# Kernel optimization log

Hardware: AMD Instinct MI355X
Metric: run time of the kernel (lower is better)

Reference implementation:

```python
import jax, jax.numpy as jnp
from jax import lax
import numpy as np

LRELU = 0.01

def conv(x, w, b=None, stride=1, pad=0):
    y = lax.conv_general_dilated(x, w, (stride, stride), [(pad, pad), (pad, pad)],
                                 dimension_numbers=('NCHW', 'OIHW', 'NCHW'))
    return y if b is None else y + b[None, :, None, None]

def deconv(x, w, b, stride=2, pad=1):
    # torch ConvTranspose2d (w: [Cin, Cout, k, k]) == lhs-dilated conv with flipped kernel
    k = w.shape[2]
    wf = jnp.transpose(jnp.flip(w, (2, 3)), (1, 0, 2, 3))  # -> OIHW
    y = lax.conv_general_dilated(x, wf, (1, 1), [(k - 1 - pad, k - 1 - pad)] * 2,
                                 lhs_dilation=(stride, stride),
                                 dimension_numbers=('NCHW', 'OIHW', 'NCHW'))
    return y + b[None, :, None, None]

def bn(x, g, b, eps=1e-5):
    # training-mode BatchNorm2d: batch statistics over (N, H, W)
    m = x.mean((0, 2, 3), keepdims=True)
    v = x.var((0, 2, 3), keepdims=True)
    return (x - m) * lax.rsqrt(v + eps) * g[None, :, None, None] + b[None, :, None, None]

def resblock(x, w1, g1, b1, w2, g2, b2):
    h = jax.nn.relu(bn(conv(x, w1, pad=1), g1, b1))
    return x + bn(conv(h, w2), g2, b2)

def vq_quantize(z, emb, beta=0.25):
    zt = jnp.transpose(z, (0, 2, 3, 1))              # [B,H,W,D]
    D = zt.shape[-1]
    flat = zt.reshape(-1, D)                         # [M,D]
    dist = ((flat ** 2).sum(1, keepdims=True) + (emb ** 2).sum(1)
            - 2.0 * flat @ emb.T)                    # [M,K]
    idx = jnp.argmin(dist, axis=1)                   # [M]
    q = emb[idx].reshape(zt.shape)                   # gather == one-hot @ emb
    loss = beta * jnp.mean((lax.stop_gradient(q) - zt) ** 2)
    q_st = zt + lax.stop_gradient(q - zt)            # straight-through estimator
    counts = jnp.zeros((emb.shape[0],), flat.dtype).at[idx].add(1.0)
    probs = counts / flat.shape[0]
    perplexity = jnp.exp(-jnp.sum(probs * jnp.log(probs + 1e-10)))
    return jnp.transpose(q_st, (0, 3, 1, 2)), loss, perplexity

def vqvae_forward(p, x):
    h = jax.nn.leaky_relu(conv(x, p['e1w'], p['e1b'], 2, 1), LRELU)
    h = jax.nn.leaky_relu(conv(h, p['e2w'], p['e2b'], 2, 1), LRELU)
    h = jax.nn.leaky_relu(conv(h, p['e3w'], p['e3b'], 1, 1), LRELU)
    h = resblock(h, p['er1w'], p['er1g'], p['er1b'], p['er2w'], p['er2g'], p['er2b'])
    h = jax.nn.leaky_relu(h, LRELU)
    encoded = jax.nn.leaky_relu(conv(h, p['e4w'], p['e4b']), LRELU)
    quantized, vq_loss, _ = vq_quantize(encoded, p['emb'])
    h = jax.nn.leaky_relu(conv(quantized, p['d1w'], p['d1b'], 1, 1), LRELU)
    h = resblock(h, p['dr1w'], p['dr1g'], p['dr1b'], p['dr2w'], p['dr2g'], p['dr2b'])
    h = jax.nn.leaky_relu(h, LRELU)
    h = jax.nn.leaky_relu(deconv(h, p['dt1w'], p['dt1b']), LRELU)
    recon = jnp.tanh(deconv(h, p['dt2w'], p['dt2b']))
    return recon, quantized, encoded, vq_loss

def setup_inputs():
    key = jax.random.key(0)
    ks = iter(jax.random.split(key, 40))
    def w(shape, s=0.05):
        return jax.random.normal(next(ks), shape, jnp.float32) * s
    D, K = 64, 512
    return {
        'x': jax.random.normal(next(ks), (64, 3, 128, 128), jnp.float32),
        'e1w': w((32, 3, 4, 4)), 'e1b': jnp.zeros((32,), jnp.float32),
        'e2w': w((64, 32, 4, 4)), 'e2b': jnp.zeros((64,), jnp.float32),
        'e3w': w((64, 64, 3, 3)), 'e3b': jnp.zeros((64,), jnp.float32),
        'er1w': w((64, 64, 3, 3)), 'er1g': jnp.ones((64,), jnp.float32), 'er1b': jnp.zeros((64,), jnp.float32),
        'er2w': w((64, 64, 1, 1)), 'er2g': jnp.ones((64,), jnp.float32), 'er2b': jnp.zeros((64,), jnp.float32),
        'e4w': w((D, 64, 1, 1)), 'e4b': jnp.zeros((D,), jnp.float32),
        'emb': jax.random.normal(next(ks), (K, D), jnp.float32),
        'd1w': w((64, D, 3, 3)), 'd1b': jnp.zeros((64,), jnp.float32),
        'dr1w': w((64, 64, 3, 3)), 'dr1g': jnp.ones((64,), jnp.float32), 'dr1b': jnp.zeros((64,), jnp.float32),
        'dr2w': w((64, 64, 1, 1)), 'dr2g': jnp.ones((64,), jnp.float32), 'dr2b': jnp.zeros((64,), jnp.float32),
        'dt1w': w((64, 32, 4, 4)), 'dt1b': jnp.zeros((32,), jnp.float32),
        'dt2w': w((32, 3, 4, 4)), 'dt2b': jnp.zeros((3,), jnp.float32),
    }

def reference(x, e1w, e1b, e2w, e2b, e3w, e3b, er1w, er1g, er1b, er2w, er2g, er2b,
              e4w, e4b, emb, d1w, d1b, dr1w, dr1g, dr1b, dr2w, dr2g, dr2b,
              dt1w, dt1b, dt2w, dt2b):
    p = dict(e1w=e1w, e1b=e1b, e2w=e2w, e2b=e2b, e3w=e3w, e3b=e3b,
             er1w=er1w, er1g=er1g, er1b=er1b, er2w=er2w, er2g=er2g, er2b=er2b,
             e4w=e4w, e4b=e4b, emb=emb, d1w=d1w, d1b=d1b,
             dr1w=dr1w, dr1g=dr1g, dr1b=dr1b, dr2w=dr2w, dr2g=dr2g, dr2b=dr2b,
             dt1w=dt1w, dt1b=dt1b, dt2w=dt2w, dt2b=dt2b)
    return vqvae_forward(p, x)
```

## Files before the change

### kernel.cpp

```cpp
#include <hip/hip_runtime.h>
#include <math.h>

#define LREL 0.01f
__device__ __forceinline__ float lrelu(float x) { return x > 0.f ? x : LREL * x; }
__device__ __forceinline__ float fast_tanh(float x) {
    x = fminf(fmaxf(x, -10.f), 10.f);
    float a = __expf(2.f * x);
    return (a - 1.f) / (a + 1.f);
}
__device__ __forceinline__ unsigned short f2bf(float f) {
    unsigned u = __float_as_uint(f);
    unsigned r = u + 0x7FFFu + ((u >> 16) & 1u);
    return (unsigned short)(r >> 16);
}
__device__ __forceinline__ float bf2f(unsigned short h) {
    return __uint_as_float(((unsigned)h) << 16);
}

typedef __attribute__((ext_vector_type(8))) short short8;
typedef __attribute__((ext_vector_type(4))) float f32x4;

__global__ void __launch_bounds__(256) conv_e1_t(
    const float* __restrict__ x, const float* __restrict__ w,
    const float* __restrict__ bias,
    unsigned short* __restrict__ outH, unsigned short* __restrict__ outL)
{
    __shared__ float lin[3][18][131];
    __shared__ float lw[3][16][16];
    int b = blockIdx.x;
    int n = b & 63, t = b >> 6;
    int rt = t & 7, cg = t >> 3;
    int tid = threadIdx.x;
    int r = tid >> 5, g = tid & 31;
    const float* inp = x + (size_t)n * 3 * 16384;

    #pragma unroll
    for (int ci = 0; ci < 3; ++ci)
        if (tid < 36) lin[ci][tid >> 1][(tid & 1) ? 129 : 0] = 0.f;
    #pragma unroll
    for (int ci = 0; ci < 3; ++ci)
        #pragma unroll
        for (int k = 0; k < 9; ++k) {
            int idx = k * 256 + tid;
            int row = idx >> 7, col = idx & 127;
            int gy = 16 * rt - 1 + row;
            float v = 0.f;
            if (gy >= 0 && gy < 128)
                v = inp[ci * 16384 + gy * 128 + col];
            lin[ci][row][col + 1] = v;
        }
    for (int i = tid; i < 768; i += 256) {
        int ci = i >> 8, rr = i & 255, co = rr >> 4, tt = rr & 15;
        lw[ci][co][tt] = w[((cg * 16 + co) * 3 + ci) * 16 + tt];
    }
    __syncthreads();

    float acc[16][2];
    #pragma unroll
    for (int co = 0; co < 16; ++co) { acc[co][0] = acc[co][1] = 0.f; }

    #pragma unroll
    for (int ci = 0; ci < 3; ++ci) {
        float win[4][6];
        #pragma unroll
        for (int ky = 0; ky < 4; ++ky)
            #pragma unroll
            for (int dx = 0; dx < 6; ++dx)
                win[ky][dx] = lin[ci][2 * r + ky][4 * g + dx];
        #pragma unroll
        for (int co = 0; co < 16; ++co) {
            #pragma unroll
            for (int ky = 0; ky < 4; ++ky)
                #pragma unroll
                for (int kx = 0; kx < 4; ++kx) {
                    float wv = lw[ci][co][ky * 4 + kx];
                    acc[co][0] = fmaf(win[ky][kx],     wv, acc[co][0]);
                    acc[co][1] = fmaf(win[ky][kx + 2], wv, acc[co][1]);
                }
        }
    }
    int oy = 8 * rt + r;
    size_t base0 = (((size_t)n * 4096 + oy * 64 + 2 * g) * 32 + cg * 16);
    unsigned h0[8], l0[8], h1[8], l1[8];
    #pragma unroll
    for (int p = 0; p < 8; ++p) {
        float bva = bias[cg * 16 + 2 * p];
        float bvb = bias[cg * 16 + 2 * p + 1];
        float va0 = lrelu(acc[2 * p][0] + bva),     vb0 = lrelu(acc[2 * p + 1][0] + bvb);
        float va1 = lrelu(acc[2 * p][1] + bva),     vb1 = lrelu(acc[2 * p + 1][1] + bvb);
        unsigned short ha0 = f2bf(va0), hb0 = f2bf(vb0);
        unsigned short ha1 = f2bf(va1), hb1 = f2bf(vb1);
        h0[p] = (unsigned)ha0 | ((unsigned)hb0 << 16);
        h1[p] = (unsigned)ha1 | ((unsigned)hb1 << 16);
        l0[p] = (unsigned)f2bf(va0 - bf2f(ha0)) | ((unsigned)f2bf(vb0 - bf2f(hb0)) << 16);
        l1[p] = (unsigned)f2bf(va1 - bf2f(ha1)) | ((unsigned)f2bf(vb1 - bf2f(hb1)) << 16);
    }
    unsigned* oH0 = (unsigned*)(outH + base0);
    unsigned* oL0 = (unsigned*)(outL + base0);
    unsigned* oH1 = (unsigned*)(outH + base0 + 32);
    unsigned* oL1 = (unsigned*)(outL + base0 + 32);
    #pragma unroll
    for (int p = 0; p < 8; ++p) {
        oH0[p] = h0[p]; oL0[p] = l0[p];
        oH1[p] = h1[p]; oL1[p] = l1[p];
    }
}

__global__ void __launch_bounds__(512) mfma_e2_k(
    const unsigned short* __restrict__ inH, const unsigned short* __restrict__ inL,
    const float* __restrict__ w, const float* __restrict__ bias,
    unsigned short* __restrict__ outH, unsigned short* __restrict__ outL)
{
    __shared__ unsigned short lEH[18][34][8], lEL[18][34][8];
    __shared__ unsigned short lOH[18][34][8], lOL[18][34][8];
    __shared__ unsigned short lwH[64][136], lwL[64][136];
    int b = blockIdx.x;
    int n = b >> 2, rq = b & 3;
    int tid = threadIdx.x;
    int wv = tid >> 6, l = tid & 63;
    int l15 = l & 15, lhi = l >> 4;

    f32x4 acc[4][2];
    #pragma unroll
    for (int ct = 0; ct < 4; ++ct)
        #pragma unroll
        for (int pt = 0; pt < 2; ++pt) {
            f32x4 z = {0.f, 0.f, 0.f, 0.f};
            acc[ct][pt] = z;
        }

    for (int cc = 0; cc < 4; ++cc) {
        __syncthreads();
        for (int i = tid; i < 1188; i += 512) {
            int row = i / 66, rem = i % 66;
            int par = rem & 1, cp = rem >> 1;
            int gy = 16 * rq - 1 + row;
            int gx = 2 * cp - 1 + par;
            uint4 vH = make_uint4(0u, 0u, 0u, 0u);
            uint4 vL = make_uint4(0u, 0u, 0u, 0u);
            if (gy >= 0 && gy < 64 && gx >= 0 && gx < 64) {
                size_t gi = (((size_t)n * 4096 + gy * 64 + gx) * 32 + cc * 8);
                vH = *(const uint4*)(inH + gi);
                vL = *(const uint4*)(inL + gi);
            }
            if (par == 0) {
                *(uint4*)&lEH[row][cp][0] = vH;
                *(uint4*)&lEL[row][cp][0] = vL;
            } else {
                *(uint4*)&lOH[row][cp][0] = vH;
                *(uint4*)&lOL[row][cp][0] = vL;
            }
        }
        for (int i = tid; i < 8192; i += 512) {
            int co = i >> 7, rr = i & 127;
            int ky = rr >> 5, kx = (rr >> 3) & 3, j = rr & 7;
            float wv0 = w[(co * 32 + cc * 8 + j) * 16 + ky * 4 + kx];
            unsigned short h = f2bf(wv0);
            lwH[co][ky * 32 + kx * 8 + j] = h;
            lwL[co][ky * 32 + kx * 8 + j] = f2bf(wv0 - bf2f(h));
        }
        __syncthreads();

        #pragma unroll
        for (int kg = 0; kg < 4; ++kg) {
            short8 bH[2], bL[2];
            int cpo = lhi >> 1;
            int row = 2 * wv + kg;
            #pragma unroll
            for (int pt = 0; pt < 2; ++pt) {
                int cpp = pt * 16 + l15 + cpo;
                if (lhi & 1) {
                    bH[pt] = *(const short8*)&lOH[row][cpp][0];
                    bL[pt] = *(const short8*)&lOL[row][cpp][0];
                } else {
                    bH[pt] = *(const short8*)&lEH[row][cpp][0];
                    bL[pt] = *(const short8*)&lEL[row][cpp][0];
                }
            }
            #pragma unroll
            for (int ct = 0; ct < 4; ++ct) {
                short8 aH = *(const short8*)&lwH[ct * 16 + l15][kg * 32 + lhi * 8];
                short8 aL = *(const short8*)&lwL[ct * 16 + l15][kg * 32 + lhi * 8];
                #pragma unroll
                for (int pt = 0; pt < 2; ++pt) {
                    acc[ct][pt] = __builtin_amdgcn_mfma_f32_16x16x32_bf16(aH, bH[pt], acc[ct][pt], 0, 0, 0);
                    acc[ct][pt] = __builtin_amdgcn_mfma_f32_16x16x32_bf16(aH, bL[pt], acc[ct][pt], 0, 0, 0);
                    acc[ct][pt] = __builtin_amdgcn_mfma_f32_16x16x32_bf16(aL, bH[pt], acc[ct][pt], 0, 0, 0);
                }
            }
        }
    }

    int oy = 8 * rq + wv;
    #pragma unroll
    for (int pt = 0; pt < 2; ++pt) {
        int ox = pt * 16 + l15;
        size_t base = (((size_t)n * 1024 + oy * 32 + ox) << 6);
        #pragma unroll
        for (int ct = 0; ct < 4; ++ct) {
            int co0 = ct * 16 + lhi * 4;
            #pragma unroll
            for (int jp = 0; jp < 2; ++jp) {
                float v0 = lrelu(acc[ct][pt][2 * jp]     + bias[co0 + 2 * jp]);
                float v1 = lrelu(acc[ct][pt][2 * jp + 1] + bias[co0 + 2 * jp + 1]);
                unsigned short h0 = f2bf(v0), h1 = f2bf(v1);
                *(unsigned*)(outH + base + co0 + 2 * jp) = (unsigned)h0 | ((unsigned)h1 << 16);
                *(unsigned*)(outL + base + co0 + 2 * jp) =
                    (unsigned)f2bf(v0 - bf2f(h0)) | ((unsigned)f2bf(v1 - bf2f(h1)) << 16);
            }
        }
    }
}

template<int IN, int ACT, int STATS>
__global__ void __launch_bounds__(256) conv1x1_t(
    const float* __restrict__ in, const float* __restrict__ res,
    const float* __restrict__ w, const float* __restrict__ bias,
    const float* __restrict__ fin, const float* __restrict__ g,
    const float* __restrict__ beta, float* __restrict__ out,
    float* __restrict__ psum, float* __restrict__ pss)
{
    __shared__ float lw[64][64];
    __shared__ float sga[64], sbb[64];
    int b = blockIdx.x;
    int n = b >> 3, pxb = b & 7;
    int tid = threadIdx.x;
    int pxg = tid & 31, cog = tid >> 5;
    for (int i = tid; i < 4096; i += 256) {
        int co = i >> 6, ci = i & 63;
        lw[ci][co] = w[co * 64 + ci];
    }
    if (IN >= 1 && tid < 64) {
        float ga = g[tid] * fin[2 * tid + 1];
        sga[tid] = ga;
        sbb[tid] = beta[tid] - fin[2 * tid] * ga;
    }
    __syncthreads();

    size_t base = (size_t)n * 65536 + pxb * 128 + pxg * 4;
    float acc[8][4];
    #pragma unroll
    for (int co = 0; co < 8; ++co) { acc[co][0]=acc[co][1]=acc[co][2]=acc[co][3]=0.f; }
    #pragma unroll 4
    for (int ci = 0; ci < 64; ++ci) {
        float4 xv = *(const float4*)(in + base + (size_t)ci * 1024);
        float x0, x1, x2, x3;
        if (IN == 1) {
            float ga = sga[ci], bb = sbb[ci];
            x0 = fmaxf(fmaf(xv.x, ga, bb), 0.f);
            x1 = fmaxf(fmaf(xv.y, ga, bb), 0.f);
            x2 = fmaxf(fmaf(xv.z, ga, bb), 0.f);
            x3 = fmaxf(fmaf(xv.w, ga, bb), 0.f);
        } else if (IN == 2) {
            float4 rv = *(const float4*)(res + base + (size_t)ci * 1024);
            float ga = sga[ci], bb = sbb[ci];
            x0 = lrelu(rv.x + fmaf(xv.x, ga, bb));
            x1 = lrelu(rv.y + fmaf(xv.y, ga, bb));
            x2 = lrelu(rv.z + fmaf(xv.z, ga, bb));
            x3 = lrelu(rv.w + fmaf(xv.w, ga, bb));
        } else {
            x0 = xv.x; x1 = xv.y; x2 = xv.z; x3 = xv.w;
        }
        const float4* wr = (const float4*)&lw[ci][cog * 8];
        float4 wa = wr[0], wb = wr[1];
        acc[0][0] = fmaf(x0, wa.x, acc[0][0]); acc[0][1] = fmaf(x1, wa.x, acc[0][1]);
        acc[0][2] = fmaf(x2, wa.x, acc[0][2]); acc[0][3] = fmaf(x3, wa.x, acc[0][3]);
        acc[1][0] = fmaf(x0, wa.y, acc[1][0]); acc[1][1] = fmaf(x1, wa.y, acc[1][1]);
        acc[1][2] = fmaf(x2, wa.y, acc[1][2]); acc[1][3] = fmaf(x3, wa.y, acc[1][3]);
        acc[2][0] = fmaf(x0, wa.z, acc[2][0]); acc[2][1] = fmaf(x1, wa.z, acc[2][1]);
        acc[2][2] = fmaf(x2, wa.z, acc[2][2]); acc[2][3] = fmaf(x3, wa.z, acc[2][3]);
        acc[3][0] = fmaf(x0, wa.w, acc[3][0]); acc[3][1] = fmaf(x1, wa.w, acc[3][1]);
        acc[3][2] = fmaf(x2, wa.w, acc[3][2]); acc[3][3] = fmaf(x3, wa.w, acc[3][3]);
        acc[4][0] = fmaf(x0, wb.x, acc[4][0]); acc[4][1] = fmaf(x1, wb.x, acc[4][1]);
        acc[4][2] = fmaf(x2, wb.x, acc[4][2]); acc[4][3] = fmaf(x3, wb.x, acc[4][3]);
        acc[5][0] = fmaf(x0, wb.y, acc[5][0]); acc[5][1] = fmaf(x1, wb.y, acc[5][1]);
        acc[5][2] = fmaf(x2, wb.y, acc[5][2]); acc[5][3] = fmaf(x3, wb.y, acc[5][3]);
        acc[6][0] = fmaf(x0, wb.z, acc[6][0]); acc[6][1] = fmaf(x1, wb.z, acc[6][1]);
        acc[6][2] = fmaf(x2, wb.z, acc[6][2]); acc[6][3] = fmaf(x3, wb.z, acc[6][3]);
        acc[7][0] = fmaf(x0, wb.w, acc[7][0]); acc[7][1] = fmaf(x1, wb.w, acc[7][1]);
        acc[7][2] = fmaf(x2, wb.w, acc[7][2]); acc[7][3] = fmaf(x3, wb.w, acc[7][3]);
    }
    #pragma unroll
    for (int co = 0; co < 8; ++co) {
        int coG = cog * 8 + co;
        float bv = bias ? bias[coG] : 0.f;
        float a0 = acc[co][0] + bv, a1 = acc[co][1] + bv, a2 = acc[co][2] + bv, a3 = acc[co][3] + bv;
        if (ACT == 1) { a0 = lrelu(a0); a1 = lrelu(a1); a2 = lrelu(a2); a3 = lrelu(a3); }
        float4 v; v.x = a0; v.y = a1; v.z = a2; v.w = a3;
        *(float4*)(out + base + (size_t)coG * 1024) = v;
        if (STATS) {
            float s = a0 + a1 + a2 + a3;
            float q = a0*a0 + a1*a1 + a2*a2 + a3*a3;
            #pragma unroll
            for (int m = 1; m < 32; m <<= 1) {
                s += __shfl_xor(s, m);
                q += __shfl_xor(q, m);
            }
            if (pxg == 0) {
                psum[(size_t)coG * 512 + n * 8 + pxb] = s;
                pss [(size_t)coG * 512 + n * 8 + pxb] = q;
            }
        }
    }
}

__global__ void bn_fin2_k(const float* __restrict__ psum, const float* __restrict__ pss,
                          float* __restrict__ fin, float invM, int cnt)
{
    __shared__ float s1[64][4], s2[64][4];
    int c = threadIdx.x >> 2, part = threadIdx.x & 3;
    int per = cnt >> 2;
    float s = 0.f, q = 0.f;
    for (int i = part * per; i < (part + 1) * per; ++i) {
        s += psum[(size_t)c * cnt + i];
        q += pss[(size_t)c * cnt + i];
    }
    s1[c][part] = s; s2[c][part] = q;
    __syncthreads();
    if (part == 0) {
        float ss = s1[c][0] + s1[c][1] + s1[c][2] + s1[c][3];
        float qq = s2[c][0] + s2[c][1] + s2[c][2] + s2[c][3];
        float mean = ss * invM;
        float var  = qq * invM - mean * mean;
        fin[2 * c] = mean;
        fin[2 * c + 1] = rsqrtf(var + 1e-5f);
    }
}

__global__ void bn_fin3_k(const float* __restrict__ psum, const float* __restrict__ pss,
                          float* __restrict__ fin, float invM)
{
    int c = threadIdx.x;
    if (c >= 64) return;
    float s = 0.f, q = 0.f;
    for (int i = 0; i < 256; ++i) { s += psum[c * 256 + i]; q += pss[c * 256 + i]; }
    float mean = s * invM;
    float var  = q * invM - mean * mean;
    fin[2 * c] = mean;
    fin[2 * c + 1] = rsqrtf(var + 1e-5f);
}

template<int MODE>
__global__ void __launch_bounds__(256) trans_k(
    const float* __restrict__ in, const float* __restrict__ fin,
    const float* __restrict__ g, const float* __restrict__ beta,
    unsigned short* __restrict__ outT)
{
    __shared__ unsigned short tt[256][68];
    __shared__ float sga[64], sbb[64];
    int b = blockIdx.x;
    int n = b >> 2, pxb = b & 3;
    int tid = threadIdx.x;
    if (MODE == 1) {
        if (tid < 64) {
            float ga = g[tid] * fin[2 * tid + 1];
            sga[tid] = ga;
            sbb[tid] = beta[tid] - fin[2 * tid] * ga;
        }
        __syncthreads();
    }
    for (int i = tid; i < 16384; i += 256) {
        int ci = i >> 8, px = i & 255;
        float v = in[((size_t)(n * 64 + ci) << 10) + pxb * 256 + px];
        if (MODE == 1) v = fmaxf(fmaf(v, sga[ci], sbb[ci]), 0.f);
        tt[px][ci] = f2bf(v);
    }
    __syncthreads();
    for (int o = tid; o < 4096; o += 256) {
        int px = o >> 4, c4 = o & 15;
        uint2 v = *(const uint2*)&tt[px][c4 * 4];
        *(uint2*)(outT + ((((size_t)n << 10) + pxb * 256 + px) << 6) + c4 * 4) = v;
    }
}

template<int INM>
__global__ void __launch_bounds__(256) trans_hl_k(
    const float* __restrict__ inA, const float* __restrict__ inB,
    const float* __restrict__ bias2,
    unsigned short* __restrict__ outH, unsigned short* __restrict__ outL)
{
    __shared__ unsigned short th[256][68];
    __shared__ unsigned short tl[256][68];
    __shared__ float sb[64];
    int b = blockIdx.x;
    int n = b >> 2, pxb = b & 3;
    int tid = threadIdx.x;
    if (INM == 1 && tid < 64) sb[tid] = bias2[tid];
    if (INM == 1) __syncthreads();
    for (int i = tid; i < 16384; i += 256) {
        int ci = i >> 8, px = i & 255;
        size_t gi = ((size_t)(n * 64 + ci) << 10) + pxb * 256 + px;
        float v = inA[gi];
        if (INM == 1) v = lrelu(v + inB[gi] + sb[ci]);
        unsigned short h = f2bf(v);
        th[px][ci] = h;
        tl[px][ci] = f2bf(v - bf2f(h));
    }
    __syncthreads();
    for (int o = tid; o < 4096; o += 256) {
        int px = o >> 4, c4 = o & 15;
        size_t oidx = ((((size_t)n << 10) + pxb * 256 + px) << 6) + c4 * 4;
        *(uint2*)(outH + oidx) = *(const uint2*)&th[px][c4 * 4];
        *(uint2*)(outL + oidx) = *(const uint2*)&tl[px][c4 * 4];
    }
}

__global__ void __launch_bounds__(256) bnres_trans_k(
    const float* __restrict__ xin, const float* __restrict__ res,
    const float* __restrict__ fin, const float* __restrict__ g,
    const float* __restrict__ beta, unsigned short* __restrict__ outT)
{
    __shared__ unsigned short tt[256][68];
    __shared__ float sga[64], sbb[64];
    int b = blockIdx.x;
    int n = b >> 2, pxb = b & 3;
    int tid = threadIdx.x;
    if (tid < 64) {
        float ga = g[tid] * fin[2 * tid + 1];
        sga[tid] = ga;
        sbb[tid] = beta[tid] - fin[2 * tid] * ga;
    }
    __syncthreads();
    for (int i = tid; i < 16384; i += 256) {
        int ci = i >> 8, px = i & 255;
        size_t gi = ((size_t)(n * 64 + ci) << 10) + pxb * 256 + px;
        float v = lrelu(res[gi] + fmaf(xin[gi], sga[ci], sbb[ci]));
        tt[px][ci] = f2bf(v);
    }
    __syncthreads();
    for (int o = tid; o < 4096; o += 256) {
        int px = o >> 4, c4 = o & 15;
        uint2 v = *(const uint2*)&tt[px][c4 * 4];
        *(uint2*)(outT + ((((size_t)n << 10) + pxb * 256 + px) << 6) + c4 * 4) = v;
    }
}

template<int ACT, int STATS>
__global__ void __launch_bounds__(256) mfma_conv3x3_k(
    const unsigned short* __restrict__ inT, const float* __restrict__ w,
    const float* __restrict__ bias, float* __restrict__ out,
    float* __restrict__ psum, float* __restrict__ pss)
{
    __shared__ unsigned short lin[10][34][40];
    __shared__ unsigned short lwA[32][296];
    __shared__ float sS[4][32], sQ[4][32];
    int b = blockIdx.x;
    int cg = b & 1, pxb = (b >> 1) & 3, n = b >> 3;
    int tid = threadIdx.x;
    int wv = tid >> 6, l = tid & 63;
    int l15 = l & 15, lhi = l >> 4;

    f32x4 acc[2][4];
    #pragma unroll
    for (int ct = 0; ct < 2; ++ct)
        #pragma unroll
        for (int bt = 0; bt < 4; ++bt) {
            f32x4 z = {0.f, 0.f, 0.f, 0.f};
            acc[ct][bt] = z;
        }

    for (int c2 = 0; c2 < 2; ++c2) {
        __syncthreads();
        for (int i = tid; i < 1360; i += 256) {
            int pos = i >> 2, q = i & 3;
            int row = pos / 34, col = pos % 34;
            int iy = pxb * 8 - 1 + row, ix = col - 1;
            uint4 v = make_uint4(0u, 0u, 0u, 0u);
            if (iy >= 0 && iy < 32 && ix >= 0 && ix < 32)
                v = *(const uint4*)(inT + ((((size_t)n << 10) + iy * 32 + ix) << 6) + c2 * 32 + q * 8);
            *(uint4*)&lin[row][col][q * 8] = v;
        }
        for (int i = tid; i < 9216; i += 256) {
            int col = i / 288, k = i % 288;
            int tap = k >> 5, cc = k & 31;
            int co = cg * 32 + col;
            lwA[col][k] = f2bf(w[(co * 64 + c2 * 32 + cc) * 9 + tap]);
        }
        __syncthreads();
        #pragma unroll
        for (int tap = 0; tap < 9; ++tap) {
            const int dy = tap / 3, dx = tap % 3;
            short8 a[2], bb[4];
            #pragma unroll
            for (int ct = 0; ct < 2; ++ct)
                a[ct] = *(const short8*)&lwA[ct * 16 + l15][tap * 32 + lhi * 8];
            #pragma unroll
            for (int bt = 0; bt < 4; ++bt) {
                int rr = 2 * wv + (bt >> 1);
                int cc0 = (bt & 1) * 16;
                bb[bt] = *(const short8*)&lin[rr + dy][cc0 + l15 + dx][lhi * 8];
            }
            #pragma unroll
            for (int ct = 0; ct < 2; ++ct)
                #pragma unroll
                for (int bt = 0; bt < 4; ++bt)
                    acc[ct][bt] = __builtin_amdgcn_mfma_f32_16x16x32_bf16(a[ct], bb[bt], acc[ct][bt], 0, 0, 0);
        }
    }

    int orow0 = pxb * 8 + 2 * wv;
    #pragma unroll
    for (int ct = 0; ct < 2; ++ct) {
        #pragma unroll
        for (int j = 0; j < 4; ++j) {
            int co_l = ct * 16 + lhi * 4 + j;
            int co = cg * 32 + co_l;
            float bv = bias ? bias[co] : 0.f;
            float s = 0.f, q = 0.f;
            #pragma unroll
            for (int bt = 0; bt < 4; ++bt) {
                float v = acc[ct][bt][j] + bv;
                if (ACT == 1) v = lrelu(v);
                int row = orow0 + (bt >> 1);
                int col = (bt & 1) * 16 + l15;
                out[(((size_t)n * 64 + co) << 10) + row * 32 + col] = v;
                if (STATS) { s += v; q = fmaf(v, v, q); }
            }
            if (STATS) {
                #pragma unroll
                for (int m = 1; m < 16; m <<= 1) {
                    s += __shfl_xor(s, m);
                    q += __shfl_xor(q, m);
                }
                if (l15 == 0) { sS[wv][co_l] = s; sQ[wv][co_l] = q; }
            }
        }
    }
    if (STATS) {
        __syncthreads();
        if (tid < 32) {
            float s = sS[0][tid] + sS[1][tid] + sS[2][tid] + sS[3][tid];
            float q = sQ[0][tid] + sQ[1][tid] + sQ[2][tid] + sQ[3][tid];
            psum[(cg * 32 + tid) * 256 + n * 4 + pxb] = s;
            pss [(cg * 32 + tid) * 256 + n * 4 + pxb] = q;
        }
    }
}

template<int ACT, int STATS>
__global__ void __launch_bounds__(256) mfma_conv3x3_hl_k(
    const unsigned short* __restrict__ inH, const unsigned short* __restrict__ inL,
    const float* __restrict__ w, const float* __restrict__ bias,
    float* __restrict__ out, float* __restrict__ psum, float* __restrict__ pss)
{
    __shared__ unsigned short linH[10][34][40];
    __shared__ unsigned short linL[10][34][40];
    __shared__ unsigned short lwH[32][296];
    __shared__ unsigned short lwL[32][296];
    __shared__ float sS[4][32], sQ[4][32];
    int b = blockIdx.x;
    int cg = b & 1, pxb = (b >> 1) & 3, n = b >> 3;
    int tid = threadIdx.x;
    int wv = tid >> 6, l = tid & 63;
    int l15 = l & 15, lhi = l >> 4;

    f32x4 acc[2][4];
    #pragma unroll
    for (int ct = 0; ct < 2; ++ct)
        #pragma unroll
        for (int bt = 0; bt < 4; ++bt) {
            f32x4 z = {0.f, 0.f, 0.f, 0.f};
            acc[ct][bt] = z;
        }

    for (int c2 = 0; c2 < 2; ++c2) {
        __syncthreads();
        for (int i = tid; i < 1360; i += 256) {
            int pos = i >> 2, q = i & 3;
            int row = pos / 34, col = pos % 34;
            int iy = pxb * 8 - 1 + row, ix = col - 1;
            uint4 vh = make_uint4(0u, 0u, 0u, 0u);
            uint4 vl = make_uint4(0u, 0u, 0u, 0u);
            if (iy >= 0 && iy < 32 && ix >= 0 && ix < 32) {
                size_t gi = ((((size_t)n << 10) + iy * 32 + ix) << 6) + c2 * 32 + q * 8;
                vh = *(const uint4*)(inH + gi);
                vl = *(const uint4*)(inL + gi);
            }
            *(uint4*)&linH[row][col][q * 8] = vh;
            *(uint4*)&linL[row][col][q * 8] = vl;
        }
        for (int i = tid; i < 9216; i += 256) {
            int col = i / 288, k = i % 288;
            int tap = k >> 5, cc = k & 31;
            int co = cg * 32 + col;
            float wv0 = w[(co * 64 + c2 * 32 + cc) * 9 + tap];
            unsigned short h = f2bf(wv0);
            lwH[col][k] = h;
            lwL[col][k] = f2bf(wv0 - bf2f(h));
        }
        __syncthreads();
        #pragma unroll
        for (int tap = 0; tap < 9; ++tap) {
            const int dy = tap / 3, dx = tap % 3;
            short8 aH[2], aL[2], bH[4], bL[4];
            #pragma unroll
            for (int ct = 0; ct < 2; ++ct) {
                aH[ct] = *(const short8*)&lwH[ct * 16 + l15][tap * 32 + lhi * 8];
                aL[ct] = *(const short8*)&lwL[ct * 16 + l15][tap * 32 + lhi * 8];
            }
            #pragma unroll
            for (int bt = 0; bt < 4; ++bt) {
                int rr = 2 * wv + (bt >> 1);
                int cc0 = (bt & 1) * 16;
                bH[bt] = *(const short8*)&linH[rr + dy][cc0 + l15 + dx][lhi * 8];
                bL[bt] = *(const short8*)&linL[rr + dy][cc0 + l15 + dx][lhi * 8];
            }
            #pragma unroll
            for (int ct = 0; ct < 2; ++ct)
                #pragma unroll
                for (int bt = 0; bt < 4; ++bt) {
                    acc[ct][bt] = __builtin_amdgcn_mfma_f32_16x16x32_bf16(aH[ct], bH[bt], acc[ct][bt], 0, 0, 0);
                    acc[ct][bt] = __builtin_amdgcn_mfma_f32_16x16x32_bf16(aH[ct], bL[bt], acc[ct][bt], 0, 0, 0);
                    acc[ct][bt] = __builtin_amdgcn_mfma_f32_16x16x32_bf16(aL[ct], bH[bt], acc[ct][bt], 0, 0, 0);
                }
        }
    }

    int orow0 = pxb * 8 + 2 * wv;
    #pragma unroll
    for (int ct = 0; ct < 2; ++ct) {
        #pragma unroll
        for (int j = 0; j < 4; ++j) {
            int co_l = ct * 16 + lhi * 4 + j;
            int co = cg * 32 + co_l;
            float bv = bias ? bias[co] : 0.f;
            float s = 0.f, q = 0.f;
            #pragma unroll
            for (int bt = 0; bt < 4; ++bt) {
                float v = acc[ct][bt][j] + bv;
                if (ACT == 1) v = lrelu(v);
                int row = orow0 + (bt >> 1);
                int col = (bt & 1) * 16 + l15;
                out[(((size_t)n * 64 + co) << 10) + row * 32 + col] = v;
                if (STATS) { s += v; q = fmaf(v, v, q); }
            }
            if (STATS) {
                #pragma unroll
                for (int m = 1; m < 16; m <<= 1) {
                    s += __shfl_xor(s, m);
                    q += __shfl_xor(q, m);
                }
                if (l15 == 0) { sS[wv][co_l] = s; sQ[wv][co_l] = q; }
            }
        }
    }
    if (STATS) {
        __syncthreads();
        if (tid < 32) {
            float s = sS[0][tid] + sS[1][tid] + sS[2][tid] + sS[3][tid];
            float q = sQ[0][tid] + sQ[1][tid] + sQ[2][tid] + sQ[3][tid];
            psum[(cg * 32 + tid) * 256 + n * 4 + pxb] = s;
            pss [(cg * 32 + tid) * 256 + n * 4 + pxb] = q;
        }
    }
}

template<int ACT, int STATS>
__global__ void __launch_bounds__(256) mfma_conv1x1_k(
    const unsigned short* __restrict__ inT, const float* __restrict__ w,
    const float* __restrict__ bias, float* __restrict__ out,
    float* __restrict__ psum, float* __restrict__ pss)
{
    __shared__ unsigned short lin[256][72];
    __shared__ unsigned short lwA[32][72];
    __shared__ float sS[4][32], sQ[4][32];
    int b = blockIdx.x;
    int cg = b & 1, pxb = (b >> 1) & 3, n = b >> 3;
    int tid = threadIdx.x;
    int wv = tid >> 6, l = tid & 63;
    int l15 = l & 15, lhi = l >> 4;

    for (int i = tid; i < 2048; i += 256) {
        int px = i >> 3, q = i & 7;
        uint4 v = *(const uint4*)(inT + ((((size_t)n << 10) + pxb * 256 + px) << 6) + q * 8);
        *(uint4*)&lin[px][q * 8] = v;
    }
    for (int i = tid; i < 2048; i += 256) {
        int col = i >> 6, ci = i & 63;
        lwA[col][ci] = f2bf(w[(cg * 32 + col) * 64 + ci]);
    }
    __syncthreads();

    f32x4 acc[2][4];
    #pragma unroll
    for (int ct = 0; ct < 2; ++ct)
        #pragma unroll
        for (int bt = 0; bt < 4; ++bt) {
            f32x4 z = {0.f, 0.f, 0.f, 0.f};
            acc[ct][bt] = z;
        }

    #pragma unroll
    for (int ks = 0; ks < 2; ++ks) {
        short8 a[2], bb[4];
        #pragma unroll
        for (int ct = 0; ct < 2; ++ct)
            a[ct] = *(const short8*)&lwA[ct * 16 + l15][ks * 32 + lhi * 8];
        #pragma unroll
        for (int bt = 0; bt < 4; ++bt)
            bb[bt] = *(const short8*)&lin[wv * 64 + bt * 16 + l15][ks * 32 + lhi * 8];
        #pragma unroll
        for (int ct = 0; ct < 2; ++ct)
            #pragma unroll
            for (int bt = 0; bt < 4; ++bt)
                acc[ct][bt] = __builtin_amdgcn_mfma_f32_16x16x32_bf16(a[ct], bb[bt], acc[ct][bt], 0, 0, 0);
    }

    #pragma unroll
    for (int ct = 0; ct < 2; ++ct) {
        #pragma unroll
        for (int j = 0; j < 4; ++j) {
            int co_l = ct * 16 + lhi * 4 + j;
            int co = cg * 32 + co_l;
            float bv = bias ? bias[co] : 0.f;
            float s = 0.f, q = 0.f;
            #pragma unroll
            for (int bt = 0; bt < 4; ++bt) {
                float v = acc[ct][bt][j] + bv;
                if (ACT == 1) v = lrelu(v);
                int px = pxb * 256 + wv * 64 + bt * 16 + l15;
                out[(((size_t)n * 64 + co) << 10) + px] = v;
                if (STATS) { s += v; q = fmaf(v, v, q); }
            }
            if (STATS) {
                #pragma unroll
                for (int m = 1; m < 16; m <<= 1) {
                    s += __shfl_xor(s, m);
                    q += __shfl_xor(q, m);
                }
                if (l15 == 0) { sS[wv][co_l] = s; sQ[wv][co_l] = q; }
            }
        }
    }
    if (STATS) {
        __syncthreads();
        if (tid < 32) {
            float s = sS[0][tid] + sS[1][tid] + sS[2][tid] + sS[3][tid];
            float q = sQ[0][tid] + sQ[1][tid] + sQ[2][tid] + sQ[3][tid];
            psum[(cg * 32 + tid) * 256 + n * 4 + pxb] = s;
            pss [(cg * 32 + tid) * 256 + n * 4 + pxb] = q;
        }
    }
}

__global__ void __launch_bounds__(256) mfma_dt1_k(
    const unsigned short* __restrict__ inT, const float* __restrict__ w,
    const float* __restrict__ bias, float* __restrict__ out)
{
    __shared__ unsigned short lin[5][34][40];
    __shared__ unsigned short lwA[2][32][136];
    int b = blockIdx.x;
    int ublk = b & 7, p_y = (b >> 3) & 1, n = b >> 4;
    int tid = threadIdx.x;
    int wv = tid >> 6, l = tid & 63;
    int l15 = l & 15, lhi = l >> 4;
    int pq = wv & 1;
    int vbase = 1 - pq;
    int ubase = ublk * 4 + (p_y == 0 ? 1 : 0);

    f32x4 acc[2][4];
    #pragma unroll
    for (int ct = 0; ct < 2; ++ct)
        #pragma unroll
        for (int bt = 0; bt < 4; ++bt) {
            f32x4 z = {0.f, 0.f, 0.f, 0.f};
            acc[ct][bt] = z;
        }

    for (int ch = 0; ch < 2; ++ch) {
        __syncthreads();
        for (int i = tid; i < 680; i += 256) {
            int rr = i / 136, rem = i % 136;
            int jc = rem >> 2, q = rem & 3;
            int gy = ubase - 1 + rr, gx = jc - 1;
            uint4 v = make_uint4(0u, 0u, 0u, 0u);
            if (gy >= 0 && gy < 32 && gx >= 0 && gx < 32)
                v = *(const uint4*)(inT + ((((size_t)n << 10) + gy * 32 + gx) << 6) + ch * 32 + q * 8);
            *(uint4*)&lin[rr][jc][q * 8] = v;
        }
        for (int i = tid; i < 8192; i += 256) {
            int pqq = i >> 12, co = (i >> 7) & 31, k = i & 127;
            int tap = k >> 5, cc = k & 31;
            int ci = ch * 32 + cc;
            int ky = p_y + 2 * (tap >> 1), kx = pqq + 2 * (tap & 1);
            lwA[pqq][co][k] = f2bf(w[((ci * 32 + co) << 4) + ky * 4 + kx]);
        }
        __syncthreads();
        #pragma unroll
        for (int ks = 0; ks < 4; ++ks) {
            int ty = ks >> 1, tx = ks & 1;
            short8 a[2], bb[4];
            #pragma unroll
            for (int ct = 0; ct < 2; ++ct)
                a[ct] = *(const short8*)&lwA[pq][ct * 16 + l15][ks * 32 + lhi * 8];
            #pragma unroll
            for (int bt = 0; bt < 4; ++bt) {
                int jloc = (wv >> 1) * 2 + (bt >> 1);
                int vloc = (bt & 1) * 16 + l15;
                bb[bt] = *(const short8*)&lin[jloc + 1 - ty][vloc + vbase + 1 - tx][lhi * 8];
            }
            #pragma unroll
            for (int ct = 0; ct < 2; ++ct)
                #pragma unroll
// ... 159 lines not shown
        float z1 = z[base + (size_t)(d + 1) * 1024];
        float q0 = eb[d], q1 = eb[d + 1];
        out_q[base + (size_t)d * 1024]       = q0;
        out_q[base + (size_t)(d + 1) * 1024] = q1;
        float d0 = q0 - z0, d1 = q1 - z1;
        lsum = fmaf(d0, d0, lsum);
        lsum = fmaf(d1, d1, lsum);
        tq32[tid][d >> 1] = (unsigned)f2bf(q0) | ((unsigned)f2bf(q1) << 16);
    }
    sh[tid] = lsum;
    __syncthreads();
    unsigned* oT = (unsigned*)outT;
    size_t m0 = (size_t)blockIdx.x * 256;
    #pragma unroll
    for (int k = 0; k < 32; ++k) {
        int j = k * 256 + tid;
        int px = j >> 5, c = j & 31;
        oT[(m0 + px) * 32 + c] = tq32[px][c];
    }
    for (int st = 128; st > 0; st >>= 1) {
        if (tid < st) sh[tid] += sh[tid + st];
        __syncthreads();
    }
    if (tid == 0) partials[blockIdx.x] = sh[0];
}

__global__ void vq_fin_k(const float* __restrict__ partials, float* __restrict__ out)
{
    __shared__ float sh[256];
    sh[threadIdx.x] = partials[threadIdx.x];
    __syncthreads();
    for (int st = 128; st > 0; st >>= 1) {
        if (threadIdx.x < st) sh[threadIdx.x] += sh[threadIdx.x + st];
        __syncthreads();
    }
    if (threadIdx.x == 0) out[0] = sh[0] * (0.25f / (65536.f * 64.f));
}

__global__ void __launch_bounds__(256) deconv_dt2_t(
    const float* __restrict__ in, const float* __restrict__ w,
    const float* __restrict__ bias, float* __restrict__ out)
{
    __shared__ float lin[8][4][67];
    __shared__ float lw[8][3][16];
    int b = blockIdx.x;
    int n = b & 63, rt = b >> 6;
    int tid = threadIdx.x;
    int r4 = tid >> 6, g = tid & 63;
    int oy = rt * 4 + r4;
    const float* inp = in + (size_t)n * 32 * 4096;
    int iy0 = 2 * rt - 1;
    int ky0 = (oy + 1) & 1;
    int iyA = ((oy + 1 - ky0) >> 1) - iy0;
    int iyB = iyA - 1;

    if (tid < 64) lin[tid >> 3][(tid >> 1) & 3][(tid & 1) ? 65 : 0] = 0.f;

    float acc[3][2];
    #pragma unroll
    for (int co = 0; co < 3; ++co) { acc[co][0] = acc[co][1] = 0.f; }

    int scol = tid & 63, srs = tid >> 6;
    for (int cic = 0; cic < 4; ++cic) {
        __syncthreads();
        {
            int gy = iy0 + srs;
            bool ok = (gy >= 0 && gy < 64);
            #pragma unroll
            for (int k = 0; k < 8; ++k) {
                float v = ok ? inp[(cic * 8 + k) * 4096 + gy * 64 + scol] : 0.f;
                lin[k][srs][scol + 1] = v;
            }
        }
        if (tid < 128) {
            int ci = tid >> 4, tt = tid & 15;
            #pragma unroll
            for (int co = 0; co < 3; ++co)
                lw[ci][co][tt] = w[((cic * 8 + ci) * 3 + co) * 16 + tt];
        }
        __syncthreads();
        #pragma unroll 2
        for (int ci = 0; ci < 8; ++ci) {
            float vA0 = lin[ci][iyA][g],     vA1 = lin[ci][iyA][g + 1], vA2 = lin[ci][iyA][g + 2];
            float vB0 = lin[ci][iyB][g],     vB1 = lin[ci][iyB][g + 1], vB2 = lin[ci][iyB][g + 2];
            #pragma unroll
            for (int co = 0; co < 3; ++co) {
                const float4* wp = (const float4*)lw[ci][co];
                float4 wA = wp[ky0];
                float4 wB = wp[ky0 + 2];
                acc[co][0] = fmaf(vA1, wA.y, fmaf(vA0, wA.w, fmaf(vB1, wB.y, fmaf(vB0, wB.w, acc[co][0]))));
                acc[co][1] = fmaf(vA2, wA.x, fmaf(vA1, wA.z, fmaf(vB2, wB.x, fmaf(vB1, wB.z, acc[co][1]))));
            }
        }
    }
    #pragma unroll
    for (int co = 0; co < 3; ++co) {
        float bv = bias[co];
        float2 v;
        v.x = fast_tanh(acc[co][0] + bv);
        v.y = fast_tanh(acc[co][1] + bv);
        *(float2*)(out + ((size_t)(n * 3 + co) * 16384) + oy * 128 + 2 * g) = v;
    }
}

extern "C" void kernel_launch(void* const* d_in, const int* in_sizes, int n_in,
                              void* d_out, int out_size, void* d_ws, size_t ws_size,
                              hipStream_t stream)
{
    const float* x    = (const float*)d_in[0];
    const float* e1w  = (const float*)d_in[1];
    const float* e1b  = (const float*)d_in[2];
    const float* e2w  = (const float*)d_in[3];
    const float* e2b  = (const float*)d_in[4];
    const float* e3w  = (const float*)d_in[5];
    const float* e3b  = (const float*)d_in[6];
    const float* er1w = (const float*)d_in[7];
    const float* er1g = (const float*)d_in[8];
    const float* er1b = (const float*)d_in[9];
    const float* er2w = (const float*)d_in[10];
    const float* er2g = (const float*)d_in[11];
    const float* er2b = (const float*)d_in[12];
    const float* e4w  = (const float*)d_in[13];
    const float* e4b  = (const float*)d_in[14];
    const float* emb  = (const float*)d_in[15];
    const float* d1w  = (const float*)d_in[16];
    const float* d1b  = (const float*)d_in[17];
    const float* dr1w = (const float*)d_in[18];
    const float* dr1g = (const float*)d_in[19];
    const float* dr1b = (const float*)d_in[20];
    const float* dr2w = (const float*)d_in[21];
    const float* dr2g = (const float*)d_in[22];
    const float* dr2b = (const float*)d_in[23];
    const float* dt1w = (const float*)d_in[24];
    const float* dt1b = (const float*)d_in[25];
    const float* dt2w = (const float*)d_in[26];
    const float* dt2b = (const float*)d_in[27];

    float* out = (float*)d_out;
    float* ws  = (float*)d_ws;

    float* B0 = ws;
    float* B1 = ws + 8388608;
    float* B2 = B1 + 4194304;
    float* B3 = B2 + 4194304;
    float* B4 = B3 + 4194304;
    float* psum   = B4 + 4194304;
    float* pss    = psum + 32768;
    float* fin    = pss + 32768;
    float* vq_part = fin + 128;
    unsigned long long* bestbuf = (unsigned long long*)(vq_part + 256);
    unsigned short* embH = (unsigned short*)(bestbuf + 65536);
    unsigned short* embL = embH + 32768;
    float* enq = (float*)(embL + 32768);

    unsigned short* e1H  = (unsigned short*)B0;
    unsigned short* e1L  = e1H + 8388608;
    unsigned short* tbuf  = (unsigned short*)B1;
    unsigned short* tbufH = (unsigned short*)B3;
    unsigned short* tbufL = (unsigned short*)B4;

    float* out_recon = out;
    float* out_q     = out + 3145728;
    float* out_e     = out + 7340032;
    float* out_loss  = out + 11534336;

    const float invM = 1.f / 65536.f;

    vq_prep_k<<<128, 256, 0, stream>>>(emb, embH, embL, enq);
    conv_e1_t<<<1024, 256, 0, stream>>>(x, e1w, e1b, e1H, e1L);
    mfma_e2_k<<<256, 512, 0, stream>>>(e1H, e1L, e2w, e2b, tbufH, tbufL);

    mfma_conv3x3_hl_k<1,0><<<512, 256, 0, stream>>>(tbufH, tbufL, e3w, e3b, B2, nullptr, nullptr);

    trans_hl_k<0><<<256, 256, 0, stream>>>(B2, nullptr, nullptr, tbufH, tbufL);
    mfma_conv3x3_hl_k<0,1><<<512, 256, 0, stream>>>(tbufH, tbufL, er1w, nullptr, B1, psum, pss);
    bn_fin3_k<<<1, 64, 0, stream>>>(psum, pss, fin, invM);

    conv1x1_t<1,0,1><<<512, 256, 0, stream>>>(B1, nullptr, er2w, nullptr, fin, er1g, er1b, B4, psum, pss);
    bn_fin2_k<<<1, 256, 0, stream>>>(psum, pss, fin, invM, 512);
    conv1x1_t<2,1,0><<<512, 256, 0, stream>>>(B4, B2, e4w, e4b, fin, er2g, er2b, out_e, nullptr, nullptr);

    vq_dist_mfma_k<<<512, 256, 0, stream>>>(out_e, embH, embL, enq, bestbuf);
    vq_combine_k<<<256, 256, 0, stream>>>(out_e, emb, bestbuf, out_q, tbuf, vq_part);
    vq_fin_k<<<1, 256, 0, stream>>>(vq_part, out_loss);

    mfma_conv3x3_k<1,0><<<512, 256, 0, stream>>>(tbuf, d1w, d1b, B2, nullptr, nullptr);

    trans_k<0><<<256, 256, 0, stream>>>(B2, nullptr, nullptr, nullptr, tbuf);
    mfma_conv3x3_k<0,1><<<512, 256, 0, stream>>>(tbuf, dr1w, nullptr, B3, psum, pss);
    bn_fin3_k<<<1, 64, 0, stream>>>(psum, pss, fin, invM);

    trans_k<1><<<256, 256, 0, stream>>>(B3, fin, dr1g, dr1b, tbuf);
    mfma_conv1x1_k<0,1><<<512, 256, 0, stream>>>(tbuf, dr2w, nullptr, B4, psum, pss);
    bn_fin3_k<<<1, 64, 0, stream>>>(psum, pss, fin, invM);

    bnres_trans_k<<<256, 256, 0, stream>>>(B4, B2, fin, dr2g, dr2b, tbuf);
    mfma_dt1_k<<<1024, 256, 0, stream>>>(tbuf, dt1w, dt1b, B0);

    deconv_dt2_t<<<2048, 256, 0, stream>>>(B0, dt2w, dt2b, out_recon);
}
```

Baseline: 485.8 us.

## Pre-pack conv weights to bf16 once and widen 3x3 conv blocks to 512 threads

Adds a weight-prep kernel that converts the e2, e3, er1, d1 and dr1 weights once into bf16 hi/lo arrays laid out the way the kernels read them. The conv kernels then copy weights into shared memory with 16-byte vector loads instead of doing strided scalar gathers and conversions in every block. The 3x3 MFMA kernels also move to 512 threads with one output row per wave, which halves per-wave accumulators and raises parallelism. This costs an extra kernel launch and more workspace, and the larger blocks may lower occupancy.

```diff
diff --git a/kernel.cpp b/kernel.cpp
--- a/kernel.cpp
+++ b/kernel.cpp
@@ -19,6 +19,43 @@
 
 typedef __attribute__((ext_vector_type(8))) short short8;
 typedef __attribute__((ext_vector_type(4))) float f32x4;
+
+__global__ void __launch_bounds__(256) wprep_k(
+    const float* __restrict__ e3w, const float* __restrict__ er1w,
+    const float* __restrict__ d1w, const float* __restrict__ dr1w,
+    const float* __restrict__ e2w,
+    unsigned short* __restrict__ e3wH, unsigned short* __restrict__ e3wL,
+    unsigned short* __restrict__ er1wH, unsigned short* __restrict__ er1wL,
+    unsigned short* __restrict__ d1wH, unsigned short* __restrict__ dr1wH,
+    unsigned short* __restrict__ e2wH, unsigned short* __restrict__ e2wL)
+{
+    int b = blockIdx.x, tid = threadIdx.x;
+    if (b < 576) {
+        int region = b / 144;
+        int idx = (b % 144) * 256 + tid;
+        int chunk = idx / 9216, r = idx % 9216;
+        int col = r / 288, k = r % 288;
+        int tap = k >> 5, cc = k & 31;
+        int cg = chunk & 1, c2 = chunk >> 1;
+        int co = cg * 32 + col, ci = c2 * 32 + cc;
+        const float* w = region == 0 ? e3w : region == 1 ? er1w : region == 2 ? d1w : dr1w;
+        float v = w[(co * 64 + ci) * 9 + tap];
+        unsigned short h = f2bf(v);
+        if (region == 0)      { e3wH[idx] = h;  e3wL[idx]  = f2bf(v - bf2f(h)); }
+        else if (region == 1) { er1wH[idx] = h; er1wL[idx] = f2bf(v - bf2f(h)); }
+        else if (region == 2) d1wH[idx] = h;
+        else                  dr1wH[idx] = h;
+    } else {
+        int idx = (b - 576) * 256 + tid;
+        int cc = idx >> 13, r = idx & 8191;
+        int co = r >> 7, k = r & 127;
+        int ky = k >> 5, kx = (k >> 3) & 3, j = k & 7;
+        float v = e2w[(co * 32 + cc * 8 + j) * 16 + ky * 4 + kx];
+        unsigned short h = f2bf(v);
+        e2wH[idx] = h;
+        e2wL[idx] = f2bf(v - bf2f(h));
+    }
+}
 
 __global__ void __launch_bounds__(256) conv_e1_t(
     const float* __restrict__ x, const float* __restrict__ w,
@@ -108,7 +145,8 @@
 
 __global__ void __launch_bounds__(512) mfma_e2_k(
     const unsigned short* __restrict__ inH, const unsigned short* __restrict__ inL,
-    const float* __restrict__ w, const float* __restrict__ bias,
+    const unsigned short* __restrict__ wpH, const unsigned short* __restrict__ wpL,
+    const float* __restrict__ bias,
     unsigned short* __restrict__ outH, unsigned short* __restrict__ outL)
 {
     __shared__ unsigned short lEH[18][34][8], lEL[18][34][8];
@@ -151,13 +189,11 @@
                 *(uint4*)&lOL[row][cp][0] = vL;
             }
         }
-        for (int i = tid; i < 8192; i += 512) {
-            int co = i >> 7, rr = i & 127;
-            int ky = rr >> 5, kx = (rr >> 3) & 3, j = rr & 7;
-            float wv0 = w[(co * 32 + cc * 8 + j) * 16 + ky * 4 + kx];
-            unsigned short h = f2bf(wv0);
-            lwH[co][ky * 32 + kx * 8 + j] = h;
-            lwL[co][ky * 32 + kx * 8 + j] = f2bf(wv0 - bf2f(h));
+        for (int i = tid; i < 1024; i += 512) {
+            int co = i >> 4, q = i & 15;
+            size_t gb = (size_t)cc * 8192 + co * 128 + q * 8;
+            *(uint4*)&lwH[co][q * 8] = *(const uint4*)(wpH + gb);
+            *(uint4*)&lwL[co][q * 8] = *(const uint4*)(wpL + gb);
         }
         __syncthreads();
 
@@ -436,32 +472,32 @@
 }
 
 template<int ACT, int STATS>
-__global__ void __launch_bounds__(256) mfma_conv3x3_k(
-    const unsigned short* __restrict__ inT, const float* __restrict__ w,
+__global__ void __launch_bounds__(512) mfma_conv3x3_k(
+    const unsigned short* __restrict__ inT, const unsigned short* __restrict__ wpH,
     const float* __restrict__ bias, float* __restrict__ out,
     float* __restrict__ psum, float* __restrict__ pss)
 {
     __shared__ unsigned short lin[10][34][40];
     __shared__ unsigned short lwA[32][296];
-    __shared__ float sS[4][32], sQ[4][32];
+    __shared__ float sS[8][32], sQ[8][32];
     int b = blockIdx.x;
     int cg = b & 1, pxb = (b >> 1) & 3, n = b >> 3;
     int tid = threadIdx.x;
     int wv = tid >> 6, l = tid & 63;
     int l15 = l & 15, lhi = l >> 4;
 
-    f32x4 acc[2][4];
+    f32x4 acc[2][2];
     #pragma unroll
     for (int ct = 0; ct < 2; ++ct)
         #pragma unroll
-        for (int bt = 0; bt < 4; ++bt) {
+        for (int bt = 0; bt < 2; ++bt) {
             f32x4 z = {0.f, 0.f, 0.f, 0.f};
             acc[ct][bt] = z;
         }
 
     for (int c2 = 0; c2 < 2; ++c2) {
         __syncthreads();
-        for (int i = tid; i < 1360; i += 256) {
+        for (int i = tid; i < 1360; i += 512) {
             int pos = i >> 2, q = i & 3;
             int row = pos / 34, col = pos % 34;
             int iy = pxb * 8 - 1 + row, ix = col - 1;
@@ -470,35 +506,31 @@
                 v = *(const uint4*)(inT + ((((size_t)n << 10) + iy * 32 + ix) << 6) + c2 * 32 + q * 8);
             *(uint4*)&lin[row][col][q * 8] = v;
         }
-        for (int i = tid; i < 9216; i += 256) {
-            int col = i / 288, k = i % 288;
-            int tap = k >> 5, cc = k & 31;
-            int co = cg * 32 + col;
-            lwA[col][k] = f2bf(w[(co * 64 + c2 * 32 + cc) * 9 + tap]);
+        for (int i = tid; i < 1152; i += 512) {
+            int col = i / 36, q = i % 36;
+            size_t gb = (size_t)(c2 * 2 + cg) * 9216 + col * 288 + q * 8;
+            *(uint4*)&lwA[col][q * 8] = *(const uint4*)(wpH + gb);
         }
         __syncthreads();
         #pragma unroll
         for (int tap = 0; tap < 9; ++tap) {
             const int dy = tap / 3, dx = tap % 3;
-            short8 a[2], bb[4];
+            short8 a[2], bb[2];
             #pragma unroll
             for (int ct = 0; ct < 2; ++ct)
                 a[ct] = *(const short8*)&lwA[ct * 16 + l15][tap * 32 + lhi * 8];
             #pragma unroll
-            for (int bt = 0; bt < 4; ++bt) {
-                int rr = 2 * wv + (bt >> 1);
-                int cc0 = (bt & 1) * 16;
-                bb[bt] = *(const short8*)&lin[rr + dy][cc0 + l15 + dx][lhi * 8];
-            }
+            for (int bt = 0; bt < 2; ++bt)
+                bb[bt] = *(const short8*)&lin[wv + dy][bt * 16 + l15 + dx][lhi * 8];
             #pragma unroll
             for (int ct = 0; ct < 2; ++ct)
                 #pragma unroll
-                for (int bt = 0; bt < 4; ++bt)
+                for (int bt = 0; bt < 2; ++bt)
                     acc[ct][bt] = __builtin_amdgcn_mfma_f32_16x16x32_bf16(a[ct], bb[bt], acc[ct][bt], 0, 0, 0);
         }
     }
 
-    int orow0 = pxb * 8 + 2 * wv;
+    int orow = pxb * 8 + wv;
     #pragma unroll
     for (int ct = 0; ct < 2; ++ct) {
         #pragma unroll
@@ -508,12 +540,11 @@
             float bv = bias ? bias[co] : 0.f;
             float s = 0.f, q = 0.f;
             #pragma unroll
-            for (int bt = 0; bt < 4; ++bt) {
+            for (int bt = 0; bt < 2; ++bt) {
                 float v = acc[ct][bt][j] + bv;
                 if (ACT == 1) v = lrelu(v);
-                int row = orow0 + (bt >> 1);
-                int col = (bt & 1) * 16 + l15;
-                out[(((size_t)n * 64 + co) << 10) + row * 32 + col] = v;
+                int col = bt * 16 + l15;
+                out[(((size_t)n * 64 + co) << 10) + orow * 32 + col] = v;
                 if (STATS) { s += v; q = fmaf(v, v, q); }
             }
             if (STATS) {
@@ -529,8 +560,9 @@
     if (STATS) {
         __syncthreads();
         if (tid < 32) {
-            float s = sS[0][tid] + sS[1][tid] + sS[2][tid] + sS[3][tid];
-            float q = sQ[0][tid] + sQ[1][tid] + sQ[2][tid] + sQ[3][tid];
+            float s = 0.f, q = 0.f;
+            #pragma unroll
+            for (int k = 0; k < 8; ++k) { s += sS[k][tid]; q += sQ[k][tid]; }
             psum[(cg * 32 + tid) * 256 + n * 4 + pxb] = s;
             pss [(cg * 32 + tid) * 256 + n * 4 + pxb] = q;
         }
@@ -538,34 +570,35 @@
 }
 
 template<int ACT, int STATS>
-__global__ void __launch_bounds__(256) mfma_conv3x3_hl_k(
+__global__ void __launch_bounds__(512) mfma_conv3x3_hl_k(
     const unsigned short* __restrict__ inH, const unsigned short* __restrict__ inL,
-    const float* __restrict__ w, const float* __restrict__ bias,
+    const unsigned short* __restrict__ wpH, const unsigned short* __restrict__ wpL,
+    const float* __restrict__ bias,
     float* __restrict__ out, float* __restrict__ psum, float* __restrict__ pss)
 {
     __shared__ unsigned short linH[10][34][40];
     __shared__ unsigned short linL[10][34][40];
     __shared__ unsigned short lwH[32][296];
     __shared__ unsigned short lwL[32][296];
-    __shared__ float sS[4][32], sQ[4][32];
+    __shared__ float sS[8][32], sQ[8][32];
     int b = blockIdx.x;
     int cg = b & 1, pxb = (b >> 1) & 3, n = b >> 3;
     int tid = threadIdx.x;
     int wv = tid >> 6, l = tid & 63;
     int l15 = l & 15, lhi = l >> 4;
 
-    f32x4 acc[2][4];
+    f32x4 acc[2][2];
     #pragma unroll
     for (int ct = 0; ct < 2; ++ct)
         #pragma unroll
-        for (int bt = 0; bt < 4; ++bt) {
+        for (int bt = 0; bt < 2; ++bt) {
             f32x4 z = {0.f, 0.f, 0.f, 0.f};
             acc[ct][bt] = z;
         }
 
     for (int c2 = 0; c2 < 2; ++c2) {
         __syncthreads();
-        for (int i = tid; i < 1360; i += 256) {
+        for (int i = tid; i < 1360; i += 512) {
             int pos = i >> 2, q = i & 3;
             int row = pos / 34, col = pos % 34;
             int iy = pxb * 8 - 1 + row, ix = col - 1;
@@ -579,36 +612,31 @@
             *(uint4*)&linH[row][col][q * 8] = vh;
             *(uint4*)&linL[row][col][q * 8] = vl;
         }
-        for (int i = tid; i < 9216; i += 256) {
-            int col = i / 288, k = i % 288;
-            int tap = k >> 5, cc = k & 31;
-            int co = cg * 32 + col;
-            float wv0 = w[(co * 64 + c2 * 32 + cc) * 9 + tap];
-            unsigned short h = f2bf(wv0);
-            lwH[col][k] = h;
-            lwL[col][k] = f2bf(wv0 - bf2f(h));
+        for (int i = tid; i < 1152; i += 512) {
+            int col = i / 36, q = i % 36;
+            size_t gb = (size_t)(c2 * 2 + cg) * 9216 + col * 288 + q * 8;
+            *(uint4*)&lwH[col][q * 8] = *(const uint4*)(wpH + gb);
+            *(uint4*)&lwL[col][q * 8] = *(const uint4*)(wpL + gb);
         }
         __syncthreads();
         #pragma unroll
         for (int tap = 0; tap < 9; ++tap) {
             const int dy = tap / 3, dx = tap % 3;
-            short8 aH[2], aL[2], bH[4], bL[4];
+            short8 aH[2], aL[2], bH[2], bL[2];
             #pragma unroll
             for (int ct = 0; ct < 2; ++ct) {
                 aH[ct] = *(const short8*)&lwH[ct * 16 + l15][tap * 32 + lhi * 8];
                 aL[ct] = *(const short8*)&lwL[ct * 16 + l15][tap * 32 + lhi * 8];
             }
             #pragma unroll
-            for (int bt = 0; bt < 4; ++bt) {
-                int rr = 2 * wv + (bt >> 1);
-                int cc0 = (bt & 1) * 16;
-                bH[bt] = *(const short8*)&linH[rr + dy][cc0 + l15 + dx][lhi * 8];
-                bL[bt] = *(const short8*)&linL[rr + dy][cc0 + l15 + dx][lhi * 8];
+            for (int bt = 0; bt < 2; ++bt) {
+                bH[bt] = *(const short8*)&linH[wv + dy][bt * 16 + l15 + dx][lhi * 8];
+                bL[bt] = *(const short8*)&linL[wv + dy][bt * 16 + l15 + dx][lhi * 8];
             }
             #pragma unroll
             for (int ct = 0; ct < 2; ++ct)
                 #pragma unroll
-                for (int bt = 0; bt < 4; ++bt) {
+                for (int bt = 0; bt < 2; ++bt) {
                     acc[ct][bt] = __builtin_amdgcn_mfma_f32_16x16x32_bf16(aH[ct], bH[bt], acc[ct][bt], 0, 0, 0);
                     acc[ct][bt] = __builtin_amdgcn_mfma_f32_16x16x32_bf16(aH[ct], bL[bt], acc[ct][bt], 0, 0, 0);
                     acc[ct][bt] = __builtin_amdgcn_mfma_f32_16x16x32_bf16(aL[ct], bH[bt], acc[ct][bt], 0, 0, 0);
@@ -616,7 +644,7 @@
         }
     }
 
-    int orow0 = pxb * 8 + 2 * wv;
+    int orow = pxb * 8 + wv;
     #pragma unroll
     for (int ct = 0; ct < 2; ++ct) {
         #pragma unroll
@@ -626,12 +654,11 @@
             float bv = bias ? bias[co] : 0.f;
             float s = 0.f, q = 0.f;
             #pragma unroll
-            for (int bt = 0; bt < 4; ++bt) {
+            for (int bt = 0; bt < 2; ++bt) {
                 float v = acc[ct][bt][j] + bv;
                 if (ACT == 1) v = lrelu(v);
-                int row = orow0 + (bt >> 1);
-                int col = (bt & 1) * 16 + l15;
-                out[(((size_t)n * 64 + co) << 10) + row * 32 + col] = v;
+                int col = bt * 16 + l15;
+                out[(((size_t)n * 64 + co) << 10) + orow * 32 + col] = v;
                 if (STATS) { s += v; q = fmaf(v, v, q); }
             }
             if (STATS) {
@@ -647,8 +674,9 @@
     if (STATS) {
         __syncthreads();
         if (tid < 32) {
-            float s = sS[0][tid] + sS[1][tid] + sS[2][tid] + sS[3][tid];
-            float q = sQ[0][tid] + sQ[1][tid] + sQ[2][tid] + sQ[3][tid];
+            float s = 0.f, q = 0.f;
+            #pragma unroll
+            for (int k = 0; k < 8; ++k) { s += sS[k][tid]; q += sQ[k][tid]; }
             psum[(cg * 32 + tid) * 256 + n * 4 + pxb] = s;
             pss [(cg * 32 + tid) * 256 + n * 4 + pxb] = q;
         }
@@ -1114,6 +1142,14 @@
     unsigned short* embH = (unsigned short*)(bestbuf + 65536);
     unsigned short* embL = embH + 32768;
     float* enq = (float*)(embL + 32768);
+    unsigned short* e3wH  = (unsigned short*)(enq + 512);
+    unsigned short* e3wL  = e3wH + 36864;
+    unsigned short* er1wH = e3wL + 36864;
+    unsigned short* er1wL = er1wH + 36864;
+    unsigned short* d1wH  = er1wL + 36864;
+    unsigned short* dr1wH = d1wH + 36864;
+    unsigned short* e2wH  = dr1wH + 36864;
+    unsigned short* e2wL  = e2wH + 32768;
 
     unsigned short* e1H  = (unsigned short*)B0;
     unsigned short* e1L  = e1H + 8388608;
@@ -1128,14 +1164,17 @@
 
     const float invM = 1.f / 65536.f;
 
+    wprep_k<<<704, 256, 0, stream>>>(e3w, er1w, d1w, dr1w, e2w,
+                                     e3wH, e3wL, er1wH, er1wL, d1wH, dr1wH, e2wH, e2wL);
     vq_prep_k<<<128, 256, 0, stream>>>(emb, embH, embL, enq);
+
     conv_e1_t<<<1024, 256, 0, stream>>>(x, e1w, e1b, e1H, e1L);
-    mfma_e2_k<<<256, 512, 0, stream>>>(e1H, e1L, e2w, e2b, tbufH, tbufL);
-
-    mfma_conv3x3_hl_k<1,0><<<512, 256, 0, stream>>>(tbufH, tbufL, e3w, e3b, B2, nullptr, nullptr);
+    mfma_e2_k<<<256, 512, 0, stream>>>(e1H, e1L, e2wH, e2wL, e2b, tbufH, tbufL);
+
+    mfma_conv3x3_hl_k<1,0><<<512, 512, 0, stream>>>(tbufH, tbufL, e3wH, e3wL, e3b, B2, nullptr, nullptr);
 
     trans_hl_k<0><<<256, 256, 0, stream>>>(B2, nullptr, nullptr, tbufH, tbufL);
-    mfma_conv3x3_hl_k<0,1><<<512, 256, 0, stream>>>(tbufH, tbufL, er1w, nullptr, B1, psum, pss);
+    mfma_conv3x3_hl_k<0,1><<<512, 512, 0, stream>>>(tbufH, tbufL, er1wH, er1wL, nullptr, B1, psum, pss);
     bn_fin3_k<<<1, 64, 0, stream>>>(psum, pss, fin, invM);
 
     conv1x1_t<1,0,1><<<512, 256, 0, stream>>>(B1, nullptr, er2w, nullptr, fin, er1g, er1b, B4, psum, pss);
@@ -1146,10 +1185,10 @@
     vq_combine_k<<<256, 256, 0, stream>>>(out_e, emb, bestbuf, out_q, tbuf, vq_part);
     vq_fin_k<<<1, 256, 0, stream>>>(vq_part, out_loss);
 
-    mfma_conv3x3_k<1,0><<<512, 256, 0, stream>>>(tbuf, d1w, d1b, B2, nullptr, nullptr);
+    mfma_conv3x3_k<1,0><<<512, 512, 0, stream>>>(tbuf, d1wH, d1b, B2, nullptr, nullptr);
 
     trans_k<0><<<256, 256, 0, stream>>>(B2, nullptr, nullptr, nullptr, tbuf);
-    mfma_conv3x3_k<0,1><<<512, 256, 0, stream>>>(tbuf, dr1w, nullptr, B3, psum, pss);
+    mfma_conv3x3_k<0,1><<<512, 512, 0, stream>>>(tbuf, dr1wH, nullptr, B3, psum, pss);
     bn_fin3_k<<<1, 64, 0, stream>>>(psum, pss, fin, invM);
 
     trans_k<1><<<256, 256, 0, stream>>>(B3, fin, dr1g, dr1b, tbuf);
```

New measurement: 444.3 us. -8.6%, faster.
